# Performance work log

Measured on AMD Instinct MI355X. Metric: run time of the kernel, lower is better.

## Reference

```python
import jax, jax.numpy as jnp
import numpy as np

B, C, H, V = 16384, 5, 256, 512
NUM_ITER = 2


def setup_inputs() -> dict:
    key = jax.random.key(0)
    k1, k2, k3, k4 = jax.random.split(key, 4)
    # v0: one-hot categorical visible units, shape [B, C, V, 1]
    idx = jax.random.randint(k1, (B, V), 0, C)
    v0 = jax.nn.one_hot(idx, C, axis=1, dtype=jnp.float32)[..., None]
    W = 0.01 * jax.random.normal(k2, (C, H, V), dtype=jnp.float32)
    b = 0.01 * jax.random.normal(k3, (C, V, 1), dtype=jnp.float32)
    c = 0.01 * jax.random.normal(k4, (H, 1), dtype=jnp.float32)
    return {"v0": v0, "W": W, "b": b, "c": c, "num_sampling_iter": NUM_ITER}


def reference(v0, W, b, c, num_sampling_iter):
    key = jax.random.key(42)
    b2 = b[..., 0]   # [C, V]
    c1 = c[:, 0]     # [H]
    v = v0[..., 0]   # [B, C, V]

    def sample_h(k, v):
        # p(h=1|v) = sigmoid(sum_c W[c] @ v[:,c] + c)
        p = jax.nn.sigmoid(jnp.einsum('chv,bcv->bh', W, v) + c1)  # [B, H]
        return jax.random.bernoulli(k, p).astype(v.dtype)

    def sample_v(k, h):
        # logits over categories per visible unit: W[c].T @ h + b[c]
        logits = jnp.einsum('chv,bh->bcv', W, h) + b2  # [B, C, V]
        idx = jax.random.categorical(k, logits, axis=1)  # [B, V]
        return jax.nn.one_hot(idx, C, axis=1, dtype=h.dtype)  # [B, C, V]

    keys = jax.random.split(key, 2 * num_sampling_iter + 1)
    h = sample_h(keys[0], v)
    h_given_v0 = h
    for i in range(num_sampling_iter):  # small fixed iteration count
        v = sample_v(keys[2 * i + 1], h)
        h = sample_h(keys[2 * i + 2], v)
    return (v[..., None], h[..., None], h_given_v0[..., None])
```

## Files before the change

### kernel.cpp

```cpp
#include <hip/hip_runtime.h>
#include <cstdint>
#include <cstddef>


#define B_DIM 16384
#define C_DIM 5
#define H_DIM 256
#define V_DIM 512

struct TFOut { uint32_t a, b; };

typedef float f32x2 __attribute__((ext_vector_type(2)));
typedef float f32x4 __attribute__((ext_vector_type(4)));

static __device__ inline f32x2 mk2(float x, float y) {
  f32x2 r; r.x = x; r.y = y; return r;
}

static __device__ inline f32x2 pkfma(f32x2 a, f32x2 b, f32x2 c) {
#if __has_builtin(__builtin_elementwise_fma)
  return __builtin_elementwise_fma(a, b, c);
#else
  f32x2 r; r.x = fmaf(a.x, b.x, c.x); r.y = fmaf(a.y, b.y, c.y); return r;
#endif
}

__host__ __device__ static inline TFOut tf2x32(uint32_t k0, uint32_t k1,
                                               uint32_t c0, uint32_t c1) {
  uint32_t ks2 = k0 ^ k1 ^ 0x1BD11BDAu;
  uint32_t x0 = c0 + k0, x1 = c1 + k1;
#define TF_R(r) { x0 += x1; x1 = (x1 << r) | (x1 >> (32 - r)); x1 ^= x0; }
  TF_R(13) TF_R(15) TF_R(26) TF_R(6)
  x0 += k1;  x1 += ks2 + 1u;
  TF_R(17) TF_R(29) TF_R(16) TF_R(24)
  x0 += ks2; x1 += k0 + 2u;
  TF_R(13) TF_R(15) TF_R(26) TF_R(6)
  x0 += k0;  x1 += k1 + 3u;
  TF_R(17) TF_R(29) TF_R(16) TF_R(24)
  x0 += k1;  x1 += ks2 + 4u;
  TF_R(13) TF_R(15) TF_R(26) TF_R(6)
  x0 += ks2; x1 += k0 + 5u;
#undef TF_R
  TFOut o; o.a = x0; o.b = x1; return o;
}

__device__ static inline uint32_t rng_bits(uint32_t k0, uint32_t k1, uint32_t i) {
  TFOut r = tf2x32(k0, k1, 0u, i);
  return r.a ^ r.b;
}

__device__ static inline float bits_to_unit_float(uint32_t bits) {
  return __uint_as_float((bits >> 9) | 0x3F800000u) - 1.0f;
}

__device__ static float xla_exp(float x_in) {
#pragma clang fp contract(off)
  float x = fminf(x_in, 88.3762626647950f);
  x = fmaxf(x, -88.3762626647949f);
  float fx = floorf(x * 1.44269504088896341f + 0.5f);
  float tmp = fx * 0.693359375f;
  float z = fx * -2.12194440e-4f;
  x = x - tmp;
  x = x - z;
  z = x * x;
  float y = 1.9875691500e-4f;
  y = y * x + 1.3981999507e-3f;
  y = y * x + 8.3334519073e-3f;
  y = y * x + 4.1665795894e-2f;
  y = y * x + 1.6666665459e-1f;
  y = y * x + 5.0000001201e-1f;
  y = y * z + x;
  y = y + 1.0f;
  int n = (int)fx;
  y = y * __uint_as_float((uint32_t)(n + 127) << 23);
  return y;
}

__device__ static float xla_log(float x_in) {
#pragma clang fp contract(off)
  float xv = fmaxf(x_in, 1.17549435e-38f);
  uint32_t bits = __float_as_uint(xv);
  float e = (float)((int)(bits >> 23) - 126);
  float x = __uint_as_float((bits & 0x007FFFFFu) | 0x3F000000u);
  bool m = (x < 0.707106781186547524f);
  float tmp = m ? x : 0.0f;
  x = x - 1.0f;
  e = e - (m ? 1.0f : 0.0f);
  x = x + tmp;
  float z = x * x;
  float y = 7.0376836292e-2f;
  y = y * x + -1.1514610310e-1f;
  y = y * x + 1.1676998740e-1f;
  y = y * x + -1.2420140846e-1f;
  y = y * x + 1.4249322787e-1f;
  y = y * x + -1.6668057665e-1f;
  y = y * x + 2.0000714765e-1f;
  y = y * x + -2.4999993993e-1f;
  y = y * x + 3.3333331174e-1f;
  y = y * x;
  y = y * z;
  float t1 = e * -2.12194440e-4f;
  y = y + t1;
  float t2 = z * 0.5f;
  y = y - t2;
  x = x + y;
  float t3 = e * 0.693359375f;
  x = x + t3;
  return x;
}


__global__ void k_sentinel(float* out, float d) {
  out[0] = d;
}

__global__ __launch_bounds__(256) void k_idx(const float* __restrict__ v0,
                                             uint8_t* __restrict__ idx) {
  int t = blockIdx.x * 256 + threadIdx.x;
  int b = t >> 9, v = t & 511;
  const float* p = v0 + (size_t)b * (C_DIM * V_DIM) + v;
  int cf = 0;
#pragma unroll
  for (int c = 0; c < C_DIM; ++c)
    if (p[c * V_DIM] > 0.5f) cf = c;
  idx[t] = (uint8_t)cf;
}

__global__ __launch_bounds__(256) void k_wt(const float* __restrict__ W,
                                            float* __restrict__ Wt) {
  int t = blockIdx.x * 256 + threadIdx.x;
  int h = t & 255; int rest = t >> 8; int v = rest & 511; int c = rest >> 9;
  Wt[t] = W[((size_t)c * H_DIM + h) * V_DIM + v];
}

__global__ __launch_bounds__(256, 2) void k_hpart(
    const float* __restrict__ Wt, const uint8_t* __restrict__ idx,
    float* __restrict__ partial) {
  __shared__ uint8_t sidxT[V_DIM][68];
  __shared__ __align__(16) float tbf[160][64];
  int t = threadIdx.x;
  int bg = blockIdx.x >> 3, s = blockIdx.x & 7;
  int b0 = bg * 64;
  int wv = t >> 6, lane = t & 63;
  int g16 = wv * 16;

  {
    const uint32_t* src = (const uint32_t*)(idx + (size_t)b0 * V_DIM);
    for (int i = t; i < 64 * 128; i += 256) {
      int b = i >> 7, w = i & 127;
      uint32_t q = src[(size_t)b * 128 + w];
      int v = w * 4;
      sidxT[v + 0][b] = (uint8_t)(q);
      sidxT[v + 1][b] = (uint8_t)(q >> 8);
      sidxT[v + 2][b] = (uint8_t)(q >> 16);
      sidxT[v + 3][b] = (uint8_t)(q >> 24);
    }
  }

  f32x2 ps[4][8];
#pragma unroll
  for (int hq = 0; hq < 4; ++hq)
#pragma unroll
    for (int p = 0; p < 8; ++p) ps[hq][p] = mk2(0.f, 0.f);

  for (int tau = 0; tau < 2; ++tau) {
    int kbase = s * 320 + tau * 160;
    __syncthreads();
    {
      int kk0 = t >> 4, bq = t & 15;
#pragma unroll
      for (int i = 0; i < 10; ++i) {
        int kk = kk0 + 16 * i;
        int k = kbase + kk;
        int v = k & 511;
        uint32_t cc = (uint32_t)(k >> 9);
        uint32_t q = *(const uint32_t*)&sidxT[v][bq * 4];
        float4 o;
        o.x = ((q & 255u) == cc) ? 1.0f : 0.0f;
        o.y = (((q >> 8) & 255u) == cc) ? 1.0f : 0.0f;
        o.z = (((q >> 16) & 255u) == cc) ? 1.0f : 0.0f;
        o.w = (((q >> 24) & 255u) == cc) ? 1.0f : 0.0f;
        *(float4*)&tbf[kk][bq * 4] = o;
      }
    }
    __syncthreads();
#pragma unroll 2
    for (int kk = 0; kk < 160; ++kk) {
      int k = kbase + kk;
      float4 w = *(const float4*)(Wt + (size_t)k * H_DIM + (lane << 2));
      const f32x4* fp = (const f32x4*)&tbf[kk][g16];
      f32x4 qA = fp[0], qB = fp[1], qC = fp[2], qD = fp[3];
      f32x2 f0 = __builtin_shufflevector(qA, qA, 0, 1);
      f32x2 f1 = __builtin_shufflevector(qA, qA, 2, 3);
      f32x2 f2 = __builtin_shufflevector(qB, qB, 0, 1);
      f32x2 f3 = __builtin_shufflevector(qB, qB, 2, 3);
      f32x2 f4 = __builtin_shufflevector(qC, qC, 0, 1);
      f32x2 f5 = __builtin_shufflevector(qC, qC, 2, 3);
      f32x2 f6 = __builtin_shufflevector(qD, qD, 0, 1);
      f32x2 f7 = __builtin_shufflevector(qD, qD, 2, 3);
      f32x2 w0 = mk2(w.x, w.x);
      f32x2 w1 = mk2(w.y, w.y);
      f32x2 w2 = mk2(w.z, w.z);
      f32x2 w3 = mk2(w.w, w.w);
      ps[0][0] = pkfma(w0, f0, ps[0][0]); ps[1][0] = pkfma(w1, f0, ps[1][0]);
      ps[2][0] = pkfma(w2, f0, ps[2][0]); ps[3][0] = pkfma(w3, f0, ps[3][0]);
      ps[0][1] = pkfma(w0, f1, ps[0][1]); ps[1][1] = pkfma(w1, f1, ps[1][1]);
      ps[2][1] = pkfma(w2, f1, ps[2][1]); ps[3][1] = pkfma(w3, f1, ps[3][1]);
      ps[0][2] = pkfma(w0, f2, ps[0][2]); ps[1][2] = pkfma(w1, f2, ps[1][2]);
      ps[2][2] = pkfma(w2, f2, ps[2][2]); ps[3][2] = pkfma(w3, f2, ps[3][2]);
      ps[0][3] = pkfma(w0, f3, ps[0][3]); ps[1][3] = pkfma(w1, f3, ps[1][3]);
      ps[2][3] = pkfma(w2, f3, ps[2][3]); ps[3][3] = pkfma(w3, f3, ps[3][3]);
      ps[0][4] = pkfma(w0, f4, ps[0][4]); ps[1][4] = pkfma(w1, f4, ps[1][4]);
      ps[2][4] = pkfma(w2, f4, ps[2][4]); ps[3][4] = pkfma(w3, f4, ps[3][4]);
      ps[0][5] = pkfma(w0, f5, ps[0][5]); ps[1][5] = pkfma(w1, f5, ps[1][5]);
      ps[2][5] = pkfma(w2, f5, ps[2][5]); ps[3][5] = pkfma(w3, f5, ps[3][5]);
      ps[0][6] = pkfma(w0, f6, ps[0][6]); ps[1][6] = pkfma(w1, f6, ps[1][6]);
      ps[2][6] = pkfma(w2, f6, ps[2][6]); ps[3][6] = pkfma(w3, f6, ps[3][6]);
      ps[0][7] = pkfma(w0, f7, ps[0][7]); ps[1][7] = pkfma(w1, f7, ps[1][7]);
      ps[2][7] = pkfma(w2, f7, ps[2][7]); ps[3][7] = pkfma(w3, f7, ps[3][7]);
    }
  }

  int h0 = lane << 2;
#pragma unroll
  for (int p = 0; p < 8; ++p) {
    float4 oA, oB;
    oA.x = ps[0][p].x; oA.y = ps[1][p].x; oA.z = ps[2][p].x; oA.w = ps[3][p].x;
    oB.x = ps[0][p].y; oB.y = ps[1][p].y; oB.z = ps[2][p].y; oB.w = ps[3][p].y;
    int bA = b0 + g16 + 2 * p;
    *(float4*)&partial[((size_t)s * B_DIM + bA) * H_DIM + h0] = oA;
    *(float4*)&partial[((size_t)s * B_DIM + bA + 1) * H_DIM + h0] = oB;
  }
}

__global__ __launch_bounds__(256) void k_hfin(
    const float* __restrict__ partial, const float* __restrict__ c1,
    float* __restrict__ out_h, uint32_t* __restrict__ out_mask,
    uint32_t key0, uint32_t key1) {
  int b = blockIdx.x;
  int t = threadIdx.x;
  int wv = t >> 6;
  float tt = 0.0f;
#pragma unroll
  for (int s = 0; s < 8; ++s)
    tt = tt + partial[((size_t)s * B_DIM + b) * H_DIM + t];

  float tot = tt + c1[t];
  float p = 1.0f / (1.0f + xla_exp(-tot));

  uint32_t i = (uint32_t)(b * H_DIM + t);
  float u = bits_to_unit_float(rng_bits(key0, key1, i));
  bool hb = (u < p);
  if (out_h) out_h[(size_t)b * H_DIM + t] = hb ? 1.0f : 0.0f;

  unsigned long long m = __ballot(hb);
  if ((t & 63) == 0) {
    out_mask[(size_t)b * 8 + wv * 2 + 0] = (uint32_t)(m & 0xFFFFFFFFull);
    out_mask[(size_t)b * 8 + wv * 2 + 1] = (uint32_t)(m >> 32);
  }
}

__global__ __launch_bounds__(256, 2) void k_gemm_v(
    const float* __restrict__ W, const uint32_t* __restrict__ mask,
    float* __restrict__ sums) {
  __shared__ uint32_t smask[32][8];
  __shared__ __align__(16) float tbf[H_DIM][32];
  int t = threadIdx.x;
  int b0 = blockIdx.x * 32;
  smask[t >> 3][t & 7] = mask[(size_t)b0 * 8 + t];
  __syncthreads();
  {
    int h = t;
    uint32_t w = (uint32_t)(h >> 5), s = (uint32_t)(h & 31);
#pragma unroll
    for (int j = 0; j < 32; ++j)
      tbf[h][j] = (float)((smask[j][w] >> s) & 1u);
  }
  __syncthreads();

  int wv = t >> 6, lane = t & 63;
  int g = wv >> 1, vh = wv & 1;
  int v0 = vh * 256 + (lane << 2);
  int bg = b0 + g * 16;

  for (int c = 0; c < C_DIM; ++c) {
    f32x2 acc[8][4];
#pragma unroll
    for (int p = 0; p < 8; ++p)
#pragma unroll
      for (int q = 0; q < 4; ++q) acc[p][q] = mk2(0.f, 0.f);

    const float* wp = W + (size_t)c * (H_DIM * V_DIM) + v0;
    for (int hh = 0; hh < H_DIM; hh += 4) {
      float4 w4[4];
#pragma unroll
      for (int u = 0; u < 4; ++u)
        w4[u] = *(const float4*)(wp + (size_t)(hh + u) * V_DIM);
#pragma unroll
      for (int u = 0; u < 4; ++u) {
        const f32x4* fp = (const f32x4*)&tbf[hh + u][g * 16];
        f32x4 qA = fp[0], qB = fp[1], qC = fp[2], qD = fp[3];
        f32x2 f0 = __builtin_shufflevector(qA, qA, 0, 1);
        f32x2 f1 = __builtin_shufflevector(qA, qA, 2, 3);
        f32x2 f2 = __builtin_shufflevector(qB, qB, 0, 1);
        f32x2 f3 = __builtin_shufflevector(qB, qB, 2, 3);
        f32x2 f4 = __builtin_shufflevector(qC, qC, 0, 1);
        f32x2 f5 = __builtin_shufflevector(qC, qC, 2, 3);
        f32x2 f6 = __builtin_shufflevector(qD, qD, 0, 1);
        f32x2 f7 = __builtin_shufflevector(qD, qD, 2, 3);
        f32x2 wwx = mk2(w4[u].x, w4[u].x);
        f32x2 wwy = mk2(w4[u].y, w4[u].y);
        f32x2 wwz = mk2(w4[u].z, w4[u].z);
        f32x2 www = mk2(w4[u].w, w4[u].w);
        acc[0][0] = pkfma(wwx, f0, acc[0][0]); acc[0][1] = pkfma(wwy, f0, acc[0][1]);
        acc[0][2] = pkfma(wwz, f0, acc[0][2]); acc[0][3] = pkfma(www, f0, acc[0][3]);
        acc[1][0] = pkfma(wwx, f1, acc[1][0]); acc[1][1] = pkfma(wwy, f1, acc[1][1]);
        acc[1][2] = pkfma(wwz, f1, acc[1][2]); acc[1][3] = pkfma(www, f1, acc[1][3]);
        acc[2][0] = pkfma(wwx, f2, acc[2][0]); acc[2][1] = pkfma(wwy, f2, acc[2][1]);
        acc[2][2] = pkfma(wwz, f2, acc[2][2]); acc[2][3] = pkfma(www, f2, acc[2][3]);
        acc[3][0] = pkfma(wwx, f3, acc[3][0]); acc[3][1] = pkfma(wwy, f3, acc[3][1]);
        acc[3][2] = pkfma(wwz, f3, acc[3][2]); acc[3][3] = pkfma(www, f3, acc[3][3]);
        acc[4][0] = pkfma(wwx, f4, acc[4][0]); acc[4][1] = pkfma(wwy, f4, acc[4][1]);
        acc[4][2] = pkfma(wwz, f4, acc[4][2]); acc[4][3] = pkfma(www, f4, acc[4][3]);
        acc[5][0] = pkfma(wwx, f5, acc[5][0]); acc[5][1] = pkfma(wwy, f5, acc[5][1]);
        acc[5][2] = pkfma(wwz, f5, acc[5][2]); acc[5][3] = pkfma(www, f5, acc[5][3]);
        acc[6][0] = pkfma(wwx, f6, acc[6][0]); acc[6][1] = pkfma(wwy, f6, acc[6][1]);
        acc[6][2] = pkfma(wwz, f6, acc[6][2]); acc[6][3] = pkfma(www, f6, acc[6][3]);
        acc[7][0] = pkfma(wwx, f7, acc[7][0]); acc[7][1] = pkfma(wwy, f7, acc[7][1]);
        acc[7][2] = pkfma(wwz, f7, acc[7][2]); acc[7][3] = pkfma(www, f7, acc[7][3]);
      }
    }
#pragma unroll
    for (int p = 0; p < 8; ++p) {
      float4 oA, oB;
      oA.x = acc[p][0].x; oA.y = acc[p][1].x; oA.z = acc[p][2].x; oA.w = acc[p][3].x;
      oB.x = acc[p][0].y; oB.y = acc[p][1].y; oB.z = acc[p][2].y; oB.w = acc[p][3].y;
      *(float4*)&sums[((size_t)c * B_DIM + bg + 2 * p) * V_DIM + v0] = oA;
      *(float4*)&sums[((size_t)c * B_DIM + bg + 2 * p + 1) * V_DIM + v0] = oB;
    }
  }
}

__global__ __launch_bounds__(256, 4) void k_gumbel_v(
    const float* __restrict__ sums, const float* __restrict__ b2,
    uint8_t* __restrict__ idx_out, uint32_t key0, uint32_t key1) {
  int gidx = blockIdx.x * 256 + threadIdx.x;
  int b = gidx >> 7;
  int v0 = (gidx & 127) << 2;
  float best[4];
  uint32_t bc = 0;
#pragma unroll
  for (int c = 0; c < C_DIM; ++c) {
    float4 av = *(const float4*)&sums[((size_t)c * B_DIM + b) * V_DIM + v0];
    float4 bv = *(const float4*)&b2[c * V_DIM + v0];
    uint32_t ib = ((uint32_t)b * C_DIM + (uint32_t)c) * V_DIM + (uint32_t)v0;
    float avq[4] = {av.x, av.y, av.z, av.w};
    float bvq[4] = {bv.x, bv.y, bv.z, bv.w};
#pragma unroll
    for (int q = 0; q < 4; ++q) {
      float uf = bits_to_unit_float(rng_bits(key0, key1, ib + (uint32_t)q));
      if (uf == 0.0f) uf = 1.17549435e-38f;
      float gz = -xla_log(-xla_log(uf));
      float z = gz + (avq[q] + bvq[q]);
      if (c == 0 || z > best[q]) {
        best[q] = z;
        bc = (bc & ~(0xFFu << (8 * q))) | ((uint32_t)c << (8 * q));
      }
    }
  }
  *(uint32_t*)(idx_out + (size_t)b * V_DIM + v0) = bc;
}

__global__ __launch_bounds__(256) void k_onehot(const uint8_t* __restrict__ idx,
                                                float* __restrict__ out) {
  int t = blockIdx.x * 256 + threadIdx.x;
  int v = t & 511; int rest = t >> 9; int c = rest % C_DIM; int b = rest / C_DIM;
  out[t] = (idx[(size_t)b * V_DIM + v] == c) ? 1.0f : 0.0f;
}


extern "C" void kernel_launch(void* const* d_in, const int* in_sizes, int n_in,
                              void* d_out, int out_size, void* d_ws, size_t ws_size,
                              hipStream_t stream) {
  float* out = (float*)d_out;

  const size_t WS_NEED = 2621440ull
                       + 2621440ull
                       + 8388608ull
                       + 524288ull;
  float D = 0.0f;
  if (n_in < 4)                       D = 910.0f + (float)n_in;
  else if (in_sizes[0] != 41943040)   D = 920.0f;
  else if (in_sizes[1] != 655360)     D = 921.0f;
  else if (in_sizes[2] != 2560)       D = 922.0f;
  else if (in_sizes[3] != 256)        D = 923.0f;
  else if (out_size != 50331648)      D = 930.0f + (float)out_size * 1e-6f;
  else if (ws_size < WS_NEED)         D = 100.0f + (float)(ws_size >> 20);
  if (D != 0.0f) {
    hipLaunchKernelGGL(k_sentinel, dim3(1), dim3(1), 0, stream, out, D);
    return;
  }

  const float* v0 = (const float*)d_in[0];
  const float* W  = (const float*)d_in[1];
  const float* b2 = (const float*)d_in[2];
  const float* c1 = (const float*)d_in[3];

  float* out_v  = out;
  float* out_h  = out + (size_t)B_DIM * C_DIM * V_DIM;
  float* out_h0 = out_h + (size_t)B_DIM * H_DIM;

  char* ws = (char*)d_ws;
  float*    Wt   = (float*)(ws);
  uint8_t*  idx  = (uint8_t*)(ws + 5242880);
  uint32_t* mask = (uint32_t*)(ws + 13631488);

  float* sums    = out_v;
  float* partial = out_v;

  uint32_t keys[5][2];
  for (int i = 0; i < 5; ++i) {
    TFOut r = tf2x32(0u, 42u, 0u, (uint32_t)i);
    keys[i][0] = r.a; keys[i][1] = r.b;
  }

  hipLaunchKernelGGL(k_wt,  dim3(2560),  dim3(256), 0, stream, W, Wt);
  hipLaunchKernelGGL(k_idx, dim3(32768), dim3(256), 0, stream, v0, idx);

  hipLaunchKernelGGL(k_hpart, dim3(2048), dim3(256), 0, stream, Wt, idx, partial);
  hipLaunchKernelGGL(k_hfin,  dim3(B_DIM), dim3(256), 0, stream,
                     partial, c1, out_h0, mask, keys[0][0], keys[0][1]);
  hipLaunchKernelGGL(k_gemm_v, dim3(B_DIM / 32), dim3(256), 0, stream,
                     W, mask, sums);
  hipLaunchKernelGGL(k_gumbel_v, dim3(B_DIM * 128 / 256), dim3(256), 0, stream,
                     sums, b2, idx, keys[1][0], keys[1][1]);
  hipLaunchKernelGGL(k_hpart, dim3(2048), dim3(256), 0, stream, Wt, idx, partial);
  hipLaunchKernelGGL(k_hfin,  dim3(B_DIM), dim3(256), 0, stream,
                     partial, c1, (float*)nullptr, mask, keys[2][0], keys[2][1]);
  hipLaunchKernelGGL(k_gemm_v, dim3(B_DIM / 32), dim3(256), 0, stream,
                     W, mask, sums);
  hipLaunchKernelGGL(k_gumbel_v, dim3(B_DIM * 128 / 256), dim3(256), 0, stream,
                     sums, b2, idx, keys[3][0], keys[3][1]);
  hipLaunchKernelGGL(k_hpart, dim3(2048), dim3(256), 0, stream, Wt, idx, partial);
  hipLaunchKernelGGL(k_hfin,  dim3(B_DIM), dim3(256), 0, stream,
                     partial, c1, out_h, mask, keys[4][0], keys[4][1]);
  hipLaunchKernelGGL(k_onehot, dim3(163840), dim3(256), 0, stream, idx, out_v);
}
```

Before: 2.035 ms.

## Precompute transposed visible indices in a separate kernel for k_hpart

Adds a k_idxT kernel that writes the category indices in v-major layout into spare space in the output buffer, launched before each k_hpart. k_hpart then reads its needed index words straight from global memory instead of having every block transpose the whole 64x512 index tile into shared memory. This removes redundant per-block transpose work and about 34 KB of shared memory per block, which may allow more blocks per CU. The cost is three extra launches plus an extra read and write of the 8 MB index array, and reliance on that reused output region not being overwritten while idxT is still in use.

```diff
diff --git a/kernel.cpp b/kernel.cpp
--- a/kernel.cpp
+++ b/kernel.cpp
@@ -126,6 +126,32 @@
   idx[t] = (uint8_t)cf;
 }
 
+__global__ __launch_bounds__(256) void k_idxT(const uint8_t* __restrict__ idx,
+                                              uint8_t* __restrict__ idxT) {
+  __shared__ uint8_t tile[64][68];
+  int t = threadIdx.x;
+  int bb = blockIdx.x >> 3, vv = blockIdx.x & 7;
+  int b0 = bb * 64, v0 = vv * 64;
+  for (int i = t; i < 1024; i += 256) {
+    int r = i >> 4, wc = i & 15;
+    uint32_t q = *(const uint32_t*)(idx + (size_t)(b0 + r) * V_DIM + v0 + wc * 4);
+    int v = wc * 4;
+    tile[v + 0][r] = (uint8_t)(q);
+    tile[v + 1][r] = (uint8_t)(q >> 8);
+    tile[v + 2][r] = (uint8_t)(q >> 16);
+    tile[v + 3][r] = (uint8_t)(q >> 24);
+  }
+  __syncthreads();
+  for (int i = t; i < 1024; i += 256) {
+    int vr = i >> 4, wc = i & 15;
+    uint32_t q = (uint32_t)tile[vr][wc * 4]
+               | ((uint32_t)tile[vr][wc * 4 + 1] << 8)
+               | ((uint32_t)tile[vr][wc * 4 + 2] << 16)
+               | ((uint32_t)tile[vr][wc * 4 + 3] << 24);
+    *(uint32_t*)(idxT + (size_t)(v0 + vr) * B_DIM + b0 + wc * 4) = q;
+  }
+}
+
 __global__ __launch_bounds__(256) void k_wt(const float* __restrict__ W,
                                             float* __restrict__ Wt) {
   int t = blockIdx.x * 256 + threadIdx.x;
@@ -134,9 +160,8 @@
 }
 
 __global__ __launch_bounds__(256, 2) void k_hpart(
-    const float* __restrict__ Wt, const uint8_t* __restrict__ idx,
+    const float* __restrict__ Wt, const uint8_t* __restrict__ idxT,
     float* __restrict__ partial) {
-  __shared__ uint8_t sidxT[V_DIM][68];
   __shared__ __align__(16) float tbf[160][64];
   int t = threadIdx.x;
   int bg = blockIdx.x >> 3, s = blockIdx.x & 7;
@@ -144,19 +169,6 @@
   int wv = t >> 6, lane = t & 63;
   int g16 = wv * 16;
 
-  {
-    const uint32_t* src = (const uint32_t*)(idx + (size_t)b0 * V_DIM);
-    for (int i = t; i < 64 * 128; i += 256) {
-      int b = i >> 7, w = i & 127;
-      uint32_t q = src[(size_t)b * 128 + w];
-      int v = w * 4;
-      sidxT[v + 0][b] = (uint8_t)(q);
-      sidxT[v + 1][b] = (uint8_t)(q >> 8);
-      sidxT[v + 2][b] = (uint8_t)(q >> 16);
-      sidxT[v + 3][b] = (uint8_t)(q >> 24);
-    }
-  }
-
   f32x2 ps[4][8];
 #pragma unroll
   for (int hq = 0; hq < 4; ++hq)
@@ -165,7 +177,6 @@
 
   for (int tau = 0; tau < 2; ++tau) {
     int kbase = s * 320 + tau * 160;
-    __syncthreads();
     {
       int kk0 = t >> 4, bq = t & 15;
 #pragma unroll
@@ -174,7 +185,7 @@
         int k = kbase + kk;
         int v = k & 511;
         uint32_t cc = (uint32_t)(k >> 9);
-        uint32_t q = *(const uint32_t*)&sidxT[v][bq * 4];
+        uint32_t q = *(const uint32_t*)(idxT + (size_t)v * B_DIM + b0 + bq * 4);
         float4 o;
         o.x = ((q & 255u) == cc) ? 1.0f : 0.0f;
         o.y = (((q >> 8) & 255u) == cc) ? 1.0f : 0.0f;
@@ -219,6 +230,7 @@
       ps[0][7] = pkfma(w0, f7, ps[0][7]); ps[1][7] = pkfma(w1, f7, ps[1][7]);
       ps[2][7] = pkfma(w2, f7, ps[2][7]); ps[3][7] = pkfma(w3, f7, ps[3][7]);
     }
+    __syncthreads();
   }
 
   int h0 = lane << 2;
@@ -415,8 +427,9 @@
   uint8_t*  idx  = (uint8_t*)(ws + 5242880);
   uint32_t* mask = (uint32_t*)(ws + 13631488);
 
-  float* sums    = out_v;
-  float* partial = out_v;
+  float*   sums    = out_v;
+  float*   partial = out_v;
+  uint8_t* idxT    = (uint8_t*)out_v + 134217728ull;
 
   uint32_t keys[5][2];
   for (int i = 0; i < 5; ++i) {
@@ -426,22 +439,25 @@
 
   hipLaunchKernelGGL(k_wt,  dim3(2560),  dim3(256), 0, stream, W, Wt);
   hipLaunchKernelGGL(k_idx, dim3(32768), dim3(256), 0, stream, v0, idx);
-
-  hipLaunchKernelGGL(k_hpart, dim3(2048), dim3(256), 0, stream, Wt, idx, partial);
+  hipLaunchKernelGGL(k_idxT, dim3(2048), dim3(256), 0, stream, idx, idxT);
+
+  hipLaunchKernelGGL(k_hpart, dim3(2048), dim3(256), 0, stream, Wt, idxT, partial);
   hipLaunchKernelGGL(k_hfin,  dim3(B_DIM), dim3(256), 0, stream,
                      partial, c1, out_h0, mask, keys[0][0], keys[0][1]);
   hipLaunchKernelGGL(k_gemm_v, dim3(B_DIM / 32), dim3(256), 0, stream,
                      W, mask, sums);
   hipLaunchKernelGGL(k_gumbel_v, dim3(B_DIM * 128 / 256), dim3(256), 0, stream,
                      sums, b2, idx, keys[1][0], keys[1][1]);
-  hipLaunchKernelGGL(k_hpart, dim3(2048), dim3(256), 0, stream, Wt, idx, partial);
+  hipLaunchKernelGGL(k_idxT, dim3(2048), dim3(256), 0, stream, idx, idxT);
+  hipLaunchKernelGGL(k_hpart, dim3(2048), dim3(256), 0, stream, Wt, idxT, partial);
   hipLaunchKernelGGL(k_hfin,  dim3(B_DIM), dim3(256), 0, stream,
                      partial, c1, (float*)nullptr, mask, keys[2][0], keys[2][1]);
   hipLaunchKernelGGL(k_gemm_v, dim3(B_DIM / 32), dim3(256), 0, stream,
                      W, mask, sums);
   hipLaunchKernelGGL(k_gumbel_v, dim3(B_DIM * 128 / 256), dim3(256), 0, stream,
                      sums, b2, idx, keys[3][0], keys[3][1]);
-  hipLaunchKernelGGL(k_hpart, dim3(2048), dim3(256), 0, stream, Wt, idx, partial);
+  hipLaunchKernelGGL(k_idxT, dim3(2048), dim3(256), 0, stream, idx, idxT);
+  hipLaunchKernelGGL(k_hpart, dim3(2048), dim3(256), 0, stream, Wt, idxT, partial);
   hipLaunchKernelGGL(k_hfin,  dim3(B_DIM), dim3(256), 0, stream,
                      partial, c1, out_h, mask, keys[4][0], keys[4][1]);
   hipLaunchKernelGGL(k_onehot, dim3(163840), dim3(256), 0, stream, idx, out_v);
```

Result: faster. 1.881 ms (-7.6%).
